# Optimization experiments

Hardware: AMD Instinct MI355X
Metric: run time of the kernel (lower is better)

The kernel has to match this reference:

```python
import jax, jax.numpy as jnp
import numpy as np

SIGMA = 1.0
N_DOCS = 10_000_000
N_SAMPLED = 8192  # n = ceil(sqrt(random_pairs)), random_pairs = 67108864


def setup_inputs() -> dict:
    key = jax.random.key(0)
    k1, k2, k3 = jax.random.split(key, 3)
    scores = jax.random.normal(k1, (N_DOCS, 1), dtype=jnp.float32)
    target = jax.random.randint(k2, (N_DOCS,), 0, 5, dtype=jnp.int32)
    random_docs = jax.random.randint(k3, (N_SAMPLED,), 0, N_DOCS, dtype=jnp.int32)
    return {"scores": scores, "target": target, "random_docs": random_docs}


def reference(scores, target, random_docs):
    # Gather sampled docs' targets and scores.
    t = target[random_docs].astype(jnp.float32)   # [n]
    s = scores[random_docs, 0]                    # [n]
    # S_ij = sign(target_i - target_j)  (the if/elif/else ladder in the source)
    S = jnp.sign(t[:, None] - t[None, :])         # [n, n]
    # Source bug preserved: z_j = s_i.detach(), so calc_p(z_i, z_j) = sigmoid(0) = 0.5 exactly.
    # lambda_ij = sigma * (0.5 * (1 - S) - 0.5). (i == j pairs contribute 0 since S = 0.)
    lam = SIGMA * (0.5 * (1.0 - S) - 0.5)         # [n, n]
    row = jnp.sum(lam, axis=1)                    # sum_j lambda_ij for each sampled i
    # Source bug preserved: lambda_i is never reset across the outer loop -> cumulative sum.
    cum = jnp.cumsum(row)                         # [n]
    # loss = sum_k cum_lambda[k] * s_{i_k}; lambdas are detached (constants w.r.t. grad).
    loss = jnp.sum(jax.lax.stop_gradient(cum) * s)
    return loss.reshape(1)
```

## Files before the change

kernel.cpp:

```cpp
#include <hip/hip_runtime.h>

#define NS  8192
#define B1  64
#define T1  128
#define REC 12

__global__ __launch_bounds__(T1) void k_gather(
    const float* __restrict__ scores,
    const int*   __restrict__ target,
    const int*   __restrict__ docs,
    float*       __restrict__ ws)
{
    const int tid  = threadIdx.x;
    const int b    = blockIdx.x;
    const int k    = b * T1 + tid;
    const int lane = tid & 63;
    const int wave = tid >> 6;

    const int   d = docs[k];
    const int   t = target[d];
    const float s = scores[d];

    float incl = s;
    #pragma unroll
    for (int off = 1; off < 64; off <<= 1) {
        const float v = __shfl_up(incl, off, 64);
        if (lane >= off) incl += v;
    }

    __shared__ float wsum[2];
    __shared__ float acc[11];
    if (lane == 63) wsum[wave] = incl;
    if (tid < 11) acc[tid] = 0.0f;
    __syncthreads();

    const float excl = incl - s + (wave == 1 ? wsum[0] : 0.0f);
    atomicAdd(&acc[t], 1.0f);
    atomicAdd(&acc[5 + t], excl);
    __syncthreads();

    if (tid < 11) {
        float v = acc[tid];
        if (tid == 10) v = wsum[0] + wsum[1];
        ws[b * REC + tid] = v;
    }
}

__global__ __launch_bounds__(64) void k_combine(
    const float* __restrict__ ws,
    float*       __restrict__ out)
{
    const int lane = threadIdx.x;

    float cnt[5], pq[5];
    #pragma unroll
    for (int v = 0; v < 5; ++v) {
        cnt[v] = ws[lane * REC + v];
        pq[v]  = ws[lane * REC + 5 + v];
    }
    const float ssum = ws[lane * REC + 10];

    float incl = ssum;
    #pragma unroll
    for (int off = 1; off < 64; off <<= 1) {
        const float v = __shfl_up(incl, off, 64);
        if (lane >= off) incl += v;
    }
    const float S_total = __shfl(incl, 63, 64);
    const float preoff  = incl - ssum;

    double Q[5], C[5];
    #pragma unroll
    for (int v = 0; v < 5; ++v) {
        Q[v] = (double)cnt[v] * (double)(S_total - preoff) - (double)pq[v];
        C[v] = (double)cnt[v];
    }

    #pragma unroll
    for (int v = 0; v < 5; ++v) {
        #pragma unroll
        for (int off = 32; off > 0; off >>= 1) {
            Q[v] += __shfl_down(Q[v], off, 64);
            C[v] += __shfl_down(C[v], off, 64);
        }
    }

    if (lane == 0) {
        double loss = 0.0;
        #pragma unroll
        for (int w = 0; w < 5; ++w) {
            double lo = 0.0, hi = 0.0;
            #pragma unroll
            for (int v = 0; v < 5; ++v) {
                if (v < w) lo += Q[v];
                if (v > w) hi += Q[v];
            }
            loss += C[w] * (lo - hi);
        }
        out[0] = (float)(0.5 * loss);
    }
}

extern "C" void kernel_launch(void* const* d_in, const int* in_sizes, int n_in,
                              void* d_out, int out_size, void* d_ws, size_t ws_size,
                              hipStream_t stream) {
    const float* scores = (const float*)d_in[0];
    const int*   target = (const int*)d_in[1];
    const int*   docs   = (const int*)d_in[2];
    float*       out    = (float*)d_out;
    float*       ws     = (float*)d_ws;

    k_gather <<<B1, T1, 0, stream>>>(scores, target, docs, ws);
    k_combine<<<1, 64, 0, stream>>>(ws, out);
}
```

Measured before the change: 11.79 us.

## Fuse gather and combine kernels via cooperative grid sync

Merges the per-block gather/partial-reduction kernel and the single-block combine kernel into one cooperative launch. A grid-wide sync separates the phases, and block 0 then does the final reduction. The aim is to remove the second kernel launch and its inter-kernel gap. In exchange it pays for a grid barrier and the overhead of a cooperative launch, which can be costly on AMD.

```diff
diff --git a/kernel.cpp b/kernel.cpp
--- a/kernel.cpp
+++ b/kernel.cpp
@@ -1,15 +1,19 @@
 #include <hip/hip_runtime.h>
+#include <hip/hip_cooperative_groups.h>
+
+namespace cg = cooperative_groups;
 
 #define NS  8192
 #define B1  64
 #define T1  128
 #define REC 12
 
-__global__ __launch_bounds__(T1) void k_gather(
+__global__ __launch_bounds__(T1) void k_fused(
     const float* __restrict__ scores,
     const int*   __restrict__ target,
     const int*   __restrict__ docs,
-    float*       __restrict__ ws)
+    float*       __restrict__ ws,
+    float*       __restrict__ out)
 {
     const int tid  = threadIdx.x;
     const int b    = blockIdx.x;
@@ -44,60 +48,58 @@
         if (tid == 10) v = wsum[0] + wsum[1];
         ws[b * REC + tid] = v;
     }
-}
 
-__global__ __launch_bounds__(64) void k_combine(
-    const float* __restrict__ ws,
-    float*       __restrict__ out)
-{
-    const int lane = threadIdx.x;
+    __threadfence();
+    cg::this_grid().sync();
 
-    float cnt[5], pq[5];
-    #pragma unroll
-    for (int v = 0; v < 5; ++v) {
-        cnt[v] = ws[lane * REC + v];
-        pq[v]  = ws[lane * REC + 5 + v];
-    }
-    const float ssum = ws[lane * REC + 10];
+    if (b == 0 && tid < 64) {
+        float cnt[5], pq[5];
+        #pragma unroll
+        for (int v = 0; v < 5; ++v) {
+            cnt[v] = ws[tid * REC + v];
+            pq[v]  = ws[tid * REC + 5 + v];
+        }
+        const float ssum = ws[tid * REC + 10];
 
-    float incl = ssum;
-    #pragma unroll
-    for (int off = 1; off < 64; off <<= 1) {
-        const float v = __shfl_up(incl, off, 64);
-        if (lane >= off) incl += v;
-    }
-    const float S_total = __shfl(incl, 63, 64);
-    const float preoff  = incl - ssum;
+        float bincl = ssum;
+        #pragma unroll
+        for (int off = 1; off < 64; off <<= 1) {
+            const float v = __shfl_up(bincl, off, 64);
+            if (lane >= off) bincl += v;
+        }
+        const float S_total = __shfl(bincl, 63, 64);
+        const float preoff  = bincl - ssum;
 
-    double Q[5], C[5];
-    #pragma unroll
-    for (int v = 0; v < 5; ++v) {
-        Q[v] = (double)cnt[v] * (double)(S_total - preoff) - (double)pq[v];
-        C[v] = (double)cnt[v];
-    }
+        double Q[5], C[5];
+        #pragma unroll
+        for (int v = 0; v < 5; ++v) {
+            Q[v] = (double)cnt[v] * (double)(S_total - preoff) - (double)pq[v];
+            C[v] = (double)cnt[v];
+        }
 
-    #pragma unroll
-    for (int v = 0; v < 5; ++v) {
         #pragma unroll
-        for (int off = 32; off > 0; off >>= 1) {
-            Q[v] += __shfl_down(Q[v], off, 64);
-            C[v] += __shfl_down(C[v], off, 64);
+        for (int v = 0; v < 5; ++v) {
+            #pragma unroll
+            for (int off = 32; off > 0; off >>= 1) {
+                Q[v] += __shfl_down(Q[v], off, 64);
+                C[v] += __shfl_down(C[v], off, 64);
+            }
         }
-    }
 
-    if (lane == 0) {
-        double loss = 0.0;
-        #pragma unroll
-        for (int w = 0; w < 5; ++w) {
-            double lo = 0.0, hi = 0.0;
+        if (tid == 0) {
+            double loss = 0.0;
             #pragma unroll
-            for (int v = 0; v < 5; ++v) {
-                if (v < w) lo += Q[v];
-                if (v > w) hi += Q[v];
+            for (int w = 0; w < 5; ++w) {
+                double lo = 0.0, hi = 0.0;
+                #pragma unroll
+                for (int v = 0; v < 5; ++v) {
+                    if (v < w) lo += Q[v];
+                    if (v > w) hi += Q[v];
+                }
+                loss += C[w] * (lo - hi);
             }
-            loss += C[w] * (lo - hi);
+            out[0] = (float)(0.5 * loss);
         }
-        out[0] = (float)(0.5 * loss);
     }
 }
 
@@ -110,6 +112,8 @@
     float*       out    = (float*)d_out;
     float*       ws     = (float*)d_ws;
 
-    k_gather <<<B1, T1, 0, stream>>>(scores, target, docs, ws);
-    k_combine<<<1, 64, 0, stream>>>(ws, out);
+    void* args[] = {(void*)&scores, (void*)&target, (void*)&docs,
+                    (void*)&ws, (void*)&out};
+    hipLaunchCooperativeKernel((void*)k_fused, dim3(B1), dim3(T1),
+                               args, 0, stream);
 }
```

Result: slower. 32.56 us (+176.2%).
